# Performance work log

Measured on AMD Instinct MI355X. Metric: run time of the kernel, lower is better.

The kernel has to match this reference:

```python
import jax, jax.numpy as jnp
import numpy as np
import math

B, S, D = 2, 2048, 2048
HQ, HKV = 16, 4            # query heads, kv heads
HD = D // HQ               # head dim = 128
REPS = HQ // HKV           # queries per kv head = 4
KVD = HKV * HD             # 512


def setup_inputs() -> dict:
    key = jax.random.key(0)
    ks = jax.random.split(key, 7)
    s = 0.02
    return {
        "hidden_states": jax.random.normal(ks[0], (B, S, D), dtype=jnp.float32),
        "Wq": jax.random.normal(ks[1], (D, D), dtype=jnp.float32) * s,
        "bq": jnp.zeros((D,), dtype=jnp.float32),
        "Wk": jax.random.normal(ks[2], (D, KVD), dtype=jnp.float32) * s,
        "bk": jnp.zeros((KVD,), dtype=jnp.float32),
        "Wv": jax.random.normal(ks[3], (D, KVD), dtype=jnp.float32) * s,
        "bv": jnp.zeros((KVD,), dtype=jnp.float32),
    }


def reference(hidden_states, Wq, bq, Wk, bk, Wv, bv):
    b, s, d = hidden_states.shape
    # Projections
    q = hidden_states @ Wq + bq                      # [B,S,D]
    k = hidden_states @ Wk + bk                      # [B,S,KVD]
    v = hidden_states @ Wv + bv                      # [B,S,KVD]
    # Split heads. torch repeat_kv_heads uses .repeat (tile), so expanded
    # head h maps to kv head (h mod HKV). Reshape q heads as (REPS, HKV)
    # so axis g indexes the kv head, matching that tiling exactly.
    q = q.reshape(b, s, HQ, HD).transpose(0, 2, 1, 3)          # [B,HQ,S,hd]
    q = q.reshape(b, REPS, HKV, s, HD)                          # [B,R,G,S,hd]
    k = k.reshape(b, s, HKV, HD).transpose(0, 2, 1, 3)          # [B,G,S,hd]
    v = v.reshape(b, s, HKV, HD).transpose(0, 2, 1, 3)          # [B,G,S,hd]
    scale = 1.0 / math.sqrt(HD)
    scores = jnp.einsum('brgsd,bgtd->brgst', q, k) * scale      # [B,R,G,S,S]
    probs = jax.nn.softmax(scores, axis=-1)
    ctx = jnp.einsum('brgst,bgtd->brgsd', probs, v)             # [B,R,G,S,hd]
    ctx = ctx.reshape(b, HQ, s, HD).transpose(0, 2, 1, 3)       # [B,S,HQ,hd]
    return ctx.reshape(b, s, HQ * HD)                            # [B,S,D]
```

## Files before the change

### kernel.cpp

```cpp
#include <hip/hip_runtime.h>
#include <hip/hip_bf16.h>

#define QSCALE   0.08838834764831845f
#define QKSCALE  0.1275174468755322f

typedef __attribute__((ext_vector_type(8))) short bh8;
typedef __attribute__((ext_vector_type(4))) float fx4;
typedef __attribute__((ext_vector_type(4))) short sh4;

typedef const __attribute__((address_space(1))) unsigned GAu;
typedef __attribute__((address_space(3))) unsigned LAu;

__device__ __forceinline__ short f2bf(float f) {
    unsigned u = __float_as_uint(f);
    unsigned r = u + 0x7fffu + ((u >> 16) & 1u);
    return (short)(r >> 16);
}

__device__ __forceinline__ unsigned pk_bf16(float x, float y) {
    union { __hip_bfloat162 h; unsigned u; } cv;
    cv.h = __float22bfloat162_rn(float2{x, y});
    return cv.u;
}

__global__ __launch_bounds__(256) void prep_all(
    const float* __restrict__ x,  short* __restrict__ xo,
    const float* __restrict__ wq, short* __restrict__ wqt,
    const float* __restrict__ wk, short* __restrict__ wkt,
    const float* __restrict__ wv, short* __restrict__ wvt) {
    __shared__ float tile[64][65];
    const int bid = blockIdx.x;
    const int tid = threadIdx.x;

    if (bid < 8192) {
        int i = bid * 256 + tid;
        float4 v = ((const float4*)x)[i];
        sh4 s;
        s.x = f2bf(v.x); s.y = f2bf(v.y); s.z = f2bf(v.z); s.w = f2bf(v.w);
        ((sh4*)xo)[i] = s;
        return;
    }

    const float* w; short* wt; int N, nb, kb;
    int t = bid - 8192;
    if (t < 1024)      { w = wq; wt = wqt; N = 2048; nb = t & 31; kb = t >> 5; }
    else if (t < 1280) { w = wk; wt = wkt; N = 512;  t -= 1024; nb = t & 7; kb = t >> 3; }
    else               { w = wv; wt = wvt; N = 512;  t -= 1280; nb = t & 7; kb = t >> 3; }
    const int K = 2048;

    {
        int c4 = tid & 15, r0 = tid >> 4;
#pragma unroll
        for (int rr = 0; rr < 4; ++rr) {
            int r = r0 + rr * 16;
            float4 v = *(const float4*)&w[(size_t)(kb * 64 + r) * N + nb * 64 + c4 * 4];
            *(float4*)&tile[r][c4 * 4] = v;
        }
    }
    __syncthreads();
    {
        int k4 = tid & 15, n0 = tid >> 4;
#pragma unroll
        for (int rr = 0; rr < 4; ++rr) {
            int n = n0 + rr * 16;
            sh4 s;
            s.x = f2bf(tile[k4 * 4 + 0][n]);
            s.y = f2bf(tile[k4 * 4 + 1][n]);
            s.z = f2bf(tile[k4 * 4 + 2][n]);
            s.w = f2bf(tile[k4 * 4 + 3][n]);
            *(sh4*)&wt[(size_t)(nb * 64 + n) * K + kb * 64 + k4 * 4] = s;
        }
    }
}

__global__ __launch_bounds__(256) void proj_gemm(
    const short* __restrict__ X,
    const short* __restrict__ WqT,
    const short* __restrict__ WkT,
    const short* __restrict__ WvT,
    const float* __restrict__ bq, const float* __restrict__ bk,
    const float* __restrict__ bv,
    short* __restrict__ Qb, short* __restrict__ Kpk, short* __restrict__ Vpk) {
    __shared__ short As0[128 * 32];
    __shared__ short As1[128 * 32];
    __shared__ short Bs0[128 * 32];
    __shared__ short Bs1[128 * 32];

    const int tid = threadIdx.x;
    const int bm = blockIdx.x;
    const int ntg = blockIdx.y;

    const short* Wm; const float* bias; int col0, kind;
    if (ntg < 16)      { Wm = WqT; bias = bq; col0 = ntg * 128;        kind = 0; }
    else if (ntg < 20) { Wm = WkT; bias = bk; col0 = (ntg - 16) * 128; kind = 1; }
    else               { Wm = WvT; bias = bv; col0 = (ntg - 20) * 128; kind = 2; }

    const int w = tid >> 6, lane = tid & 63, quad = lane >> 4, l16 = lane & 15;

    fx4 acc[2][8];
#pragma unroll
    for (int i = 0; i < 2; ++i)
#pragma unroll
        for (int j = 0; j < 8; ++j) acc[i][j] = fx4{0.f, 0.f, 0.f, 0.f};

    const int srow = w * 16 + (lane >> 2);
    const int scol = (((lane & 3) ^ ((lane >> 2) & 3)) * 8);
    const short* Ag = X + (size_t)(bm * 128 + srow) * 2048 + scol;
    const short* Bg = Wm + (size_t)(col0 + srow) * 2048 + scol;
    const int stoff = w * 512;

    const int fchunk = (quad ^ (l16 & 3)) * 8;
    const int aoff0 = (w * 32 + l16) * 32 + fchunk;
    const int aoff1 = aoff0 + 512;
    const int boff  = l16 * 32 + fchunk;

    const short* pA00 = As0 + aoff0;  const short* pA01 = As0 + aoff1;
    const short* pA10 = As1 + aoff0;  const short* pA11 = As1 + aoff1;
    const short* pB0  = Bs0 + boff;   const short* pB1  = Bs1 + boff;

#define PG_STAGE(AsD, BsD, ktile)                                               \
    do {                                                                        \
        const int k0_ = (ktile) * 32;                                           \
        _Pragma("unroll")                                                       \
        for (int j = 0; j < 2; ++j) {                                           \
            __builtin_amdgcn_global_load_lds(                                   \
                (GAu*)(Ag + (size_t)(j * 64) * 2048 + k0_),                     \
                (LAu*)(AsD + stoff + j * 2048), 16, 0, 0);                      \
            __builtin_amdgcn_global_load_lds(                                   \
                (GAu*)(Bg + (size_t)(j * 64) * 2048 + k0_),                     \
                (LAu*)(BsD + stoff + j * 2048), 16, 0, 0);                      \
        }                                                                       \
    } while (0)

#define PG_COMPUTE(pA0_, pA1_, pB_)                                             \
    do {                                                                        \
        bh8 af0 = *(const bh8*)(pA0_);                                          \
        bh8 af1 = *(const bh8*)(pA1_);                                          \
        _Pragma("unroll")                                                       \
        for (int nt = 0; nt < 8; ++nt) {                                        \
            bh8 bf = *(const bh8*)((pB_) + nt * 512);                           \
            acc[0][nt] = __builtin_amdgcn_mfma_f32_16x16x32_bf16(af0, bf, acc[0][nt], 0, 0, 0); \
            acc[1][nt] = __builtin_amdgcn_mfma_f32_16x16x32_bf16(af1, bf, acc[1][nt], 0, 0, 0); \
        }                                                                       \
    } while (0)

    PG_STAGE(As0, Bs0, 0);
    __syncthreads();

    for (int kt = 0; kt < 64; kt += 2) {
        PG_STAGE(As1, Bs1, kt + 1);
        PG_COMPUTE(pA00, pA01, pB0);
        __syncthreads();

        if (kt < 62) PG_STAGE(As0, Bs0, kt + 2);
        PG_COMPUTE(pA10, pA11, pB1);
        __syncthreads();
    }
#undef PG_STAGE
#undef PG_COMPUTE

#pragma unroll
    for (int mt = 0; mt < 2; ++mt) {
        int srow2 = bm * 128 + w * 32 + mt * 16 + quad * 4;
#pragma unroll
        for (int nt = 0; nt < 8; ++nt) {
            int c = col0 + nt * 16 + l16;
            float bval = bias[c];
#pragma unroll
            for (int r = 0; r < 4; ++r) {
                int sg = srow2 + r;
                int b = sg >> 11, s = sg & 2047;
                float v = acc[mt][nt][r] + bval;
                int hd = c & 127;
                if (kind == 0) {
                    v *= QKSCALE;
                    int h = c >> 7;
                    Qb[(((size_t)(b * 16 + h) * 2048 + s) << 7) + hd] = f2bf(v);
                } else if (kind == 1) {
                    int g = c >> 7;
                    int kt32 = s >> 5, u = s & 31;
                    int nti = (u >> 2) & 1, fl16 = (u >> 3) * 4 + (u & 3);
                    int ks = hd >> 5, qd = (hd >> 3) & 3, j = hd & 7;
                    size_t frag = (((size_t)(b * 4 + g) * 64 + kt32) * 8 + nti * 4 + ks);
                    Kpk[frag * 512 + (qd * 16 + fl16) * 8 + j] = f2bf(v);
                } else {
                    int g = c >> 7;
                    int ktt = s >> 6, tl = s & 63;
                    int ts = tl >> 5, qd = (tl >> 3) & 3, j = tl & 7;
                    int fnt = hd >> 4, fl16 = hd & 15;
                    size_t frag = (((size_t)(b * 4 + g) * 32 + ktt) * 16 + fnt * 2 + ts);
                    Vpk[frag * 512 + (qd * 16 + fl16) * 8 + j] = f2bf(v);
                }
            }
        }
    }
}

__global__ __launch_bounds__(128, 2) void attn(
    const short* __restrict__ Qb,
    const short* __restrict__ Kpk,
    const short* __restrict__ Vpk,
    float* __restrict__ out) {
    __shared__ short Ks0[8 * 512];
    __shared__ short Ks1[8 * 512];
    __shared__ short Vs0[8 * 512];
    __shared__ short Vs1[8 * 512];

    const int bid = blockIdx.x;
    const int gb = bid & 7;
    const int rep = (bid >> 3) & 3;
    const int qt = bid >> 5;
    const int b = gb >> 2, g = gb & 3;
    const int h = rep * 4 + g;
    const int tid = threadIdx.x, w = tid >> 6, lane = tid & 63;
    const int quad = lane >> 4, l16 = lane & 15;

    bh8 qf[2][4];
#pragma unroll
    for (int rg = 0; rg < 2; ++rg) {
        int s = qt * 64 + w * 32 + rg * 16 + l16;
        const short* qp = Qb + (((size_t)(b * 16 + h) * 2048 + s) << 7);
#pragma unroll
        for (int ks = 0; ks < 4; ++ks)
            qf[rg][ks] = *(const bh8*)(qp + ks * 32 + quad * 8);
    }

    const short* kbase = Kpk + ((size_t)gb * 32) * 8192;
    const short* vbase = Vpk + ((size_t)gb * 32) * 8192;

    const short* pK0 = Ks0 + lane * 8;
    const short* pK1 = Ks1 + lane * 8;
    const short* pV0 = Vs0 + lane * 8;
    const short* pV1 = Vs1 + lane * 8;

    fx4 ctx[2][8];
#pragma unroll
    for (int rg = 0; rg < 2; ++rg)
#pragma unroll
        for (int j = 0; j < 8; ++j) ctx[rg][j] = fx4{0.f, 0.f, 0.f, 0.f};
    float l_part[2] = {0.f, 0.f};

#define AT_BARRIER()  asm volatile("s_waitcnt lgkmcnt(0)\n\ts_barrier" ::: "memory")
#define AT_VM(N)      asm volatile("s_waitcnt vmcnt(" #N ")" ::: "memory")

#define AT_STAGE(KsD, VsD, kn)                                                  \
    do {                                                                        \
        const short* kp_ = kbase + (size_t)(kn) * 4096;                         \
        const short* vp_ = vbase + (size_t)((kn) >> 1) * 8192 + ((kn) & 1) * 512;\
        _Pragma("unroll")                                                       \
        for (int i = 0; i < 4; ++i) {                                           \
            int f = w * 4 + i;                                                  \
            __builtin_amdgcn_global_load_lds((GAu*)(kp_ + f * 512 + lane * 8),  \
                                             (LAu*)(KsD + f * 512), 16, 0, 0);  \
            __builtin_amdgcn_global_load_lds((GAu*)(vp_ + (size_t)f * 1024 + lane * 8),\
                                             (LAu*)(VsD + f * 512), 16, 0, 0);  \
        }                                                                       \
    } while (0)

#define AT_COMPUTE(pKC, pVC)                                                    \
    do {                                                                        \
        fx4 sc[2][2];                                                           \
        sc[0][0] = fx4{0.f, 0.f, 0.f, 0.f}; sc[0][1] = fx4{0.f, 0.f, 0.f, 0.f}; \
        sc[1][0] = fx4{0.f, 0.f, 0.f, 0.f}; sc[1][1] = fx4{0.f, 0.f, 0.f, 0.f}; \
        __builtin_amdgcn_s_setprio(1);                                          \
        _Pragma("unroll")                                                       \
        for (int nti = 0; nti < 2; ++nti) {                                     \
            _Pragma("unroll")                                                   \
            for (int ks = 0; ks < 4; ++ks) {                                    \
                bh8 kf = *(const bh8*)((pKC) + (nti * 4 + ks) * 512);           \
                sc[0][nti] = __builtin_amdgcn_mfma_f32_16x16x32_bf16(kf, qf[0][ks], sc[0][nti], 0, 0, 0); \
                sc[1][nti] = __builtin_amdgcn_mfma_f32_16x16x32_bf16(kf, qf[1][ks], sc[1][nti], 0, 0, 0); \
            }                                                                   \
        }                                                                       \
        __builtin_amdgcn_s_setprio(0);                                          \
        bh8 pa[2];                                                              \
        _Pragma("unroll")                                                       \
        for (int rg = 0; rg < 2; ++rg) {                                        \
            float e0 = __builtin_amdgcn_exp2f(sc[rg][0][0]);                    \
            float e1 = __builtin_amdgcn_exp2f(sc[rg][0][1]);                    \
            float e2 = __builtin_amdgcn_exp2f(sc[rg][0][2]);                    \
            float e3 = __builtin_amdgcn_exp2f(sc[rg][0][3]);                    \
            float e4 = __builtin_amdgcn_exp2f(sc[rg][1][0]);                    \
            float e5 = __builtin_amdgcn_exp2f(sc[rg][1][1]);                    \
            float e6 = __builtin_amdgcn_exp2f(sc[rg][1][2]);                    \
            float e7 = __builtin_amdgcn_exp2f(sc[rg][1][3]);                    \
            l_part[rg] += ((e0 + e1) + (e2 + e3)) + ((e4 + e5) + (e6 + e7));    \
            unsigned a[4];                                                      \
            a[0] = pk_bf16(e0, e1);                                             \
            a[1] = pk_bf16(e2, e3);                                             \
            a[2] = pk_bf16(e4, e5);                                             \
            a[3] = pk_bf16(e6, e7);                                             \
            pa[rg] = *(const bh8*)a;                                            \
        }                                                                       \
        __builtin_amdgcn_s_setprio(1);                                          \
        _Pragma("unroll")                                                       \
        for (int nt = 0; nt < 8; ++nt) {                                        \
            bh8 vf = *(const bh8*)((pVC) + nt * 512);                           \
            ctx[0][nt] = __builtin_amdgcn_mfma_f32_16x16x32_bf16(pa[0], vf, ctx[0][nt], 0, 0, 0); \
            ctx[1][nt] = __builtin_amdgcn_mfma_f32_16x16x32_bf16(pa[1], vf, ctx[1][nt], 0, 0, 0); \
        }                                                                       \
        __builtin_amdgcn_s_setprio(0);                                          \
    } while (0)

    AT_STAGE(Ks0, Vs0, 0);
    AT_STAGE(Ks1, Vs1, 1);
    AT_VM(0);
    AT_BARRIER();

    for (int kt = 0; kt < 62; kt += 2) {
        AT_COMPUTE(pK0, pV0);
        AT_BARRIER();
        AT_STAGE(Ks0, Vs0, kt + 2);
        AT_VM(8);
        AT_BARRIER();
        AT_COMPUTE(pK1, pV1);
        AT_BARRIER();
        AT_STAGE(Ks1, Vs1, kt + 3);
        AT_VM(8);
        AT_BARRIER();
    }
    AT_COMPUTE(pK0, pV0);
    AT_VM(0);
    AT_BARRIER();
    AT_COMPUTE(pK1, pV1);
#undef AT_STAGE
#undef AT_COMPUTE
#undef AT_BARRIER
#undef AT_VM

#pragma unroll
    for (int rg = 0; rg < 2; ++rg) {
        float lsum = l_part[rg];
        lsum += __shfl_xor(lsum, 16);
        lsum += __shfl_xor(lsum, 32);
        int srow = qt * 64 + w * 32 + rg * 16 + quad * 4;
#pragma unroll
        for (int r = 0; r < 4; ++r) {
            float inv = 1.f / __shfl(lsum, quad * 4 + r);
            size_t rowoff = ((size_t)b * 2048 + (srow + r)) * 2048 + h * 128;
#pragma unroll
            for (int nt = 0; nt < 8; ++nt)
                out[rowoff + nt * 16 + l16] = ctx[rg][nt][r] * inv;
        }
    }
}

extern "C" void kernel_launch(void* const* d_in, const int* in_sizes, int n_in,
                              void* d_out, int out_size, void* d_ws, size_t ws_size,
                              hipStream_t stream) {
    const float* hs = (const float*)d_in[0];
    const float* Wq = (const float*)d_in[1];
    const float* bq = (const float*)d_in[2];
    const float* Wk = (const float*)d_in[3];
    const float* bk = (const float*)d_in[4];
    const float* Wv = (const float*)d_in[5];
    const float* bv = (const float*)d_in[6];
    float* out = (float*)d_out;

    char* ws = (char*)d_ws;
    short* Xbf = (short*)(ws);
    short* WqT = (short*)(ws + 16777216);
    short* WkT = (short*)(ws + 25165824);
    short* WvT = (short*)(ws + 27262976);
    short* Qb  = (short*)(ws + 29360128);
    short* Kpk = (short*)(ws + 46137344);
    short* Vpk = (short*)(ws + 50331648);

    prep_all<<<9728, 256, 0, stream>>>(hs, Xbf, Wq, WqT, Wk, WkT, Wv, WvT);
    proj_gemm<<<dim3(32, 24), 256, 0, stream>>>(Xbf, WqT, WkT, WvT, bq, bk, bv,
                                                Qb, Kpk, Vpk);
    attn<<<1024, 128, 0, stream>>>(Qb, Kpk, Vpk, out);
}
```

Before: 263.0 us.

## Software-pipeline PV MFMA one tile behind QK to overlap exp with matmul

Restructures the attention inner loop so the P·V MFMAs for the previous KV tile are issued right after the current tile's QK^T MFMAs, before the exp/softmax math. V fragments are loaded into registers at the start of each tile and held in ping-pong register arrays across the barrier, and an epilogue drains the final tile. The goal is to let exp2 and bf16 packing overlap with matrix-core work instead of stalling on a serial dependency. The cost is about 16 extra bh8 registers plus the carried probabilities, which raises register pressure and may reduce occupancy.

```diff
diff --git a/kernel.cpp b/kernel.cpp
--- a/kernel.cpp
+++ b/kernel.cpp
@@ -240,6 +240,12 @@
         for (int j = 0; j < 8; ++j) ctx[rg][j] = fx4{0.f, 0.f, 0.f, 0.f};
     float l_part[2] = {0.f, 0.f};
 
+    const bh8 z8 = bh8{0, 0, 0, 0, 0, 0, 0, 0};
+    bh8 paP[2] = {z8, z8};
+    bh8 vfA[8], vfB[8];
+#pragma unroll
+    for (int f = 0; f < 8; ++f) { vfA[f] = z8; vfB[f] = z8; }
+
 #define AT_BARRIER()  asm volatile("s_waitcnt lgkmcnt(0)\n\ts_barrier" ::: "memory")
 #define AT_VM(N)      asm volatile("s_waitcnt vmcnt(" #N ")" ::: "memory")
 
@@ -257,8 +263,11 @@
         }                                                                       \
     } while (0)
 
-#define AT_COMPUTE(pKC, pVC)                                                    \
+#define AT_COMPUTE(pKC, pVC, vfC, vfP)                                          \
     do {                                                                        \
+        _Pragma("unroll")                                                       \
+        for (int nt = 0; nt < 8; ++nt)                                          \
+            vfC[nt] = *(const bh8*)((pVC) + nt * 512);                          \
         fx4 sc[2][2];                                                           \
         sc[0][0] = fx4{0.f, 0.f, 0.f, 0.f}; sc[0][1] = fx4{0.f, 0.f, 0.f, 0.f}; \
         sc[1][0] = fx4{0.f, 0.f, 0.f, 0.f}; sc[1][1] = fx4{0.f, 0.f, 0.f, 0.f}; \
@@ -272,8 +281,12 @@
                 sc[1][nti] = __builtin_amdgcn_mfma_f32_16x16x32_bf16(kf, qf[1][ks], sc[1][nti], 0, 0, 0); \
             }                                                                   \
         }                                                                       \
+        _Pragma("unroll")                                                       \
+        for (int nt = 0; nt < 8; ++nt) {                                        \
+            ctx[0][nt] = __builtin_amdgcn_mfma_f32_16x16x32_bf16(paP[0], vfP[nt], ctx[0][nt], 0, 0, 0); \
+            ctx[1][nt] = __builtin_amdgcn_mfma_f32_16x16x32_bf16(paP[1], vfP[nt], ctx[1][nt], 0, 0, 0); \
+        }                                                                       \
         __builtin_amdgcn_s_setprio(0);                                          \
-        bh8 pa[2];                                                              \
         _Pragma("unroll")                                                       \
         for (int rg = 0; rg < 2; ++rg) {                                        \
             float e0 = __builtin_amdgcn_exp2f(sc[rg][0][0]);                    \
@@ -290,16 +303,8 @@
             a[1] = pk_bf16(e2, e3);                                             \
             a[2] = pk_bf16(e4, e5);                                             \
             a[3] = pk_bf16(e6, e7);                                             \
-            pa[rg] = *(const bh8*)a;                                            \
-        }                                                                       \
-        __builtin_amdgcn_s_setprio(1);                                          \
-        _Pragma("unroll")                                                       \
-        for (int nt = 0; nt < 8; ++nt) {                                        \
-            bh8 vf = *(const bh8*)((pVC) + nt * 512);                           \
-            ctx[0][nt] = __builtin_amdgcn_mfma_f32_16x16x32_bf16(pa[0], vf, ctx[0][nt], 0, 0, 0); \
-            ctx[1][nt] = __builtin_amdgcn_mfma_f32_16x16x32_bf16(pa[1], vf, ctx[1][nt], 0, 0, 0); \
-        }                                                                       \
-        __builtin_amdgcn_s_setprio(0);                                          \
+            paP[rg] = *(const bh8*)a;                                           \
+        }                                                                       \
     } while (0)
 
     AT_STAGE(Ks0, Vs0, 0);
@@ -308,21 +313,26 @@
     AT_BARRIER();
 
     for (int kt = 0; kt < 62; kt += 2) {
-        AT_COMPUTE(pK0, pV0);
+        AT_COMPUTE(pK0, pV0, vfA, vfB);
         AT_BARRIER();
         AT_STAGE(Ks0, Vs0, kt + 2);
         AT_VM(8);
         AT_BARRIER();
-        AT_COMPUTE(pK1, pV1);
+        AT_COMPUTE(pK1, pV1, vfB, vfA);
         AT_BARRIER();
         AT_STAGE(Ks1, Vs1, kt + 3);
         AT_VM(8);
         AT_BARRIER();
     }
-    AT_COMPUTE(pK0, pV0);
+    AT_COMPUTE(pK0, pV0, vfA, vfB);
     AT_VM(0);
     AT_BARRIER();
-    AT_COMPUTE(pK1, pV1);
+    AT_COMPUTE(pK1, pV1, vfB, vfA);
+#pragma unroll
+    for (int nt = 0; nt < 8; ++nt) {
+        ctx[0][nt] = __builtin_amdgcn_mfma_f32_16x16x32_bf16(paP[0], vfB[nt], ctx[0][nt], 0, 0, 0);
+        ctx[1][nt] = __builtin_amdgcn_mfma_f32_16x16x32_bf16(paP[1], vfB[nt], ctx[1][nt], 0, 0, 0);
+    }
 #undef AT_STAGE
 #undef AT_COMPUTE
 #undef AT_BARRIER
```

Measured after the change: 258.0 us. About the same (-1.9%).
